# Optimization experiments

Measured on AMD Instinct MI355X. Metric: run time of the kernel, lower is better.

## Reference

```python
import jax, jax.numpy as jnp
import numpy as np

N_STREAMS = 4
HIDDEN = 1024
SINKHORN_ITERS = 20
TAU = 0.05
EPS = 1e-6
RMS_EPS = 1e-8


def rms_norm(x, weight):
    # x: [T, d] fp32
    rms = jnp.mean(x * x, axis=-1, keepdims=True)
    return x * jax.lax.rsqrt(rms + RMS_EPS) * weight


def sinkhorn_log(logits, n_iters=SINKHORN_ITERS, tau=TAU):
    # logits: [T, n, n] -> doubly-stochastic [T, n, n]
    Z = logits / tau
    u0 = jnp.zeros(Z.shape[:-1], Z.dtype)  # [T, n]
    v0 = jnp.zeros_like(u0)

    def body(i, uv):
        u, v = uv
        u = -jax.nn.logsumexp(Z + v[..., None, :], axis=-1)
        v = -jax.nn.logsumexp(Z + u[..., :, None], axis=-2)
        return (u, v)

    u, v = jax.lax.fori_loop(0, n_iters, body, (u0, v0))
    return jnp.exp(Z + u[..., :, None] + v[..., None, :])


def setup_inputs() -> dict:
    key = jax.random.key(0)
    ks = jax.random.split(key, 6)
    d = N_STREAMS * HIDDEN
    x_streams = jax.random.normal(ks[0], (4, 2048, N_STREAMS, HIDDEN), dtype=jnp.float32)
    scale = 1.0 / np.sqrt(d)
    return {
        "x_streams": x_streams,
        "rms_weight": jnp.ones((d,), jnp.float32),
        "W_pre": jax.random.normal(ks[1], (N_STREAMS, d), jnp.float32) * scale,
        "W_post": jax.random.normal(ks[2], (N_STREAMS, d), jnp.float32) * scale,
        "W_res": jax.random.normal(ks[3], (N_STREAMS * N_STREAMS, d), jnp.float32) * scale,
        "bias_pre": jnp.zeros((N_STREAMS,), jnp.float32),
        "bias_post": jnp.zeros((N_STREAMS,), jnp.float32),
        "bias_res": jnp.zeros((N_STREAMS * N_STREAMS,), jnp.float32),
        "alpha_pre": jnp.full((1,), 0.01, jnp.float32),
        "alpha_post": jnp.full((1,), 0.01, jnp.float32),
        "alpha_res": jnp.full((1,), 0.01, jnp.float32),
        "W_sub": jax.random.normal(ks[4], (HIDDEN, HIDDEN), jnp.float32) * (1.0 / np.sqrt(HIDDEN)),
    }


def reference(x_streams, rms_weight, W_pre, W_post, W_res, bias_pre, bias_post,
              bias_res, alpha_pre, alpha_post, alpha_res, W_sub):
    B, S, n, C = x_streams.shape
    d = n * C
    x_flat = x_streams.reshape(B * S, d).astype(jnp.float32)
    x_norm = rms_norm(x_flat, rms_weight)

    H_pre = jax.nn.sigmoid(alpha_pre * (x_norm @ W_pre.T) + bias_pre)        # [T, n]
    H_post = 2.0 * jax.nn.sigmoid(alpha_post * (x_norm @ W_post.T) + bias_post)
    H_res = sinkhorn_log((alpha_res * (x_norm @ W_res.T) + bias_res).reshape(B * S, n, n))

    H_pre = H_pre.reshape(B, S, n)
    H_post = H_post.reshape(B, S, n)
    H_res = H_res.reshape(B, S, n, n)

    H_pre_w = H_pre / (jnp.sum(H_pre, axis=-1, keepdims=True) + EPS)
    H_post_w = H_post / (jnp.sum(H_post, axis=-1, keepdims=True) + EPS)

    # pre-aggregate streams -> single stream
    x_layer = jnp.einsum('bsnc,bsn->bsc', x_streams, H_pre_w)
    # sublayer: bias-free linear
    y = x_layer @ W_sub.T                                                    # [B, S, C]
    # broadcast sublayer output back to streams
    y_expanded = H_post_w[..., None] * y[:, :, None, :]                      # [B, S, n, C]
    # doubly-stochastic residual stream mixing
    x_mixed = jnp.einsum('bsic,bsoi->bsoc', x_streams, H_res)
    return x_mixed + y_expanded
```

## Files before the change

kernel.cpp:

```cpp
#include <hip/hip_runtime.h>

#define NTOK 8192
#define D 4096
#define CH 1024

typedef __attribute__((ext_vector_type(8))) short short8v;
typedef __attribute__((ext_vector_type(4))) float float4v;
typedef __attribute__((ext_vector_type(4))) unsigned short ushort4v;

static __device__ __forceinline__ unsigned short f2bf(float f) {
  unsigned int u = __float_as_uint(f);
  u += 0x7fff + ((u >> 16) & 1);
  return (unsigned short)(u >> 16);
}

static __device__ __forceinline__ void async_cp16(const void* g, void* l) {
  __builtin_amdgcn_global_load_lds((__attribute__((address_space(1))) void*)g,
                                   (__attribute__((address_space(3))) void*)l,
                                   16, 0, 0);
}

__global__ __launch_bounds__(512, 4) void gates_kernel(
    const float* __restrict__ x, const float* __restrict__ rms_w,
    const float* __restrict__ Wpre, const float* __restrict__ Wpost,
    const float* __restrict__ Wres, const float* __restrict__ bpre,
    const float* __restrict__ bpost, const float* __restrict__ bres,
    const float* __restrict__ apre, const float* __restrict__ apost,
    const float* __restrict__ ares, const float* __restrict__ Wsub,
    unsigned short* __restrict__ Wb, float* __restrict__ gates_out,
    unsigned short* __restrict__ xlayer) {
  __shared__ float xbuf[4][4096];
  __shared__ float logits_lds[4][24];
  __shared__ float sq_lds[4];
  __shared__ float s_lds[4];
  __shared__ float hpre_lds[4][4];

  const int tid = threadIdx.x;
  const int lane = tid & 63;
  const int w = tid >> 6;
  const int tok0 = blockIdx.x * 4;

  {
    const int t = w >> 1;
    const int c0 = (w & 1) * 2048;
    const float* src = x + (size_t)(tok0 + t) * D + c0 + lane * 4;
#pragma unroll
    for (int j = 0; j < 8; ++j)
      async_cp16(src + j * 256, (void*)&xbuf[t][c0 + j * 256]);
  }

  if (blockIdx.x < 1024) {
    int i = blockIdx.x * 1024 + tid * 2;
    float2 v = *(const float2*)(Wsub + i);
    unsigned int packed = (unsigned int)f2bf(v.x) | ((unsigned int)f2bf(v.y) << 16);
    *(unsigned int*)(Wb + i) = packed;
  }

  const float* Wp[3];
#pragma unroll
  for (int g = 0; g < 3; ++g) {
    int gg = w * 3 + g;
    Wp[g] = (gg < 4) ? (Wpre + gg * D)
          : (gg < 8) ? (Wpost + (gg - 4) * D)
                     : (Wres + (gg - 8) * D);
  }

  float acc[3][4];
#pragma unroll
  for (int g = 0; g < 3; ++g)
#pragma unroll
    for (int t = 0; t < 4; ++t) acc[g][t] = 0.f;
  float sq = 0.f;

  __syncthreads();

#pragma unroll 4
  for (int chk = 0; chk < 16; ++chk) {
    const int cb = chk * 256 + lane * 4;
    float4 w4[3];
#pragma unroll
    for (int g = 0; g < 3; ++g) w4[g] = *(const float4*)(Wp[g] + cb);
    float4 r4 = *(const float4*)(rms_w + cb);
#pragma unroll
    for (int t = 0; t < 4; ++t) {
      float4 xv = *(const float4*)(&xbuf[t][cb]);
      if (w == (t << 1))
        sq += xv.x * xv.x + xv.y * xv.y + xv.z * xv.z + xv.w * xv.w;
      float4 xr;
      xr.x = xv.x * r4.x; xr.y = xv.y * r4.y; xr.z = xv.z * r4.z; xr.w = xv.w * r4.w;
#pragma unroll
      for (int g = 0; g < 3; ++g)
        acc[g][t] += xr.x * w4[g].x + xr.y * w4[g].y + xr.z * w4[g].z + xr.w * w4[g].w;
    }
  }

#pragma unroll
  for (int g = 0; g < 3; ++g)
#pragma unroll
    for (int t = 0; t < 4; ++t) {
      float v = acc[g][t];
      for (int off = 32; off > 0; off >>= 1) v += __shfl_xor(v, off, 64);
      if (lane == 0) logits_lds[t][w * 3 + g] = v;
    }
  if ((w & 1) == 0) {
    float v = sq;
    for (int off = 32; off > 0; off >>= 1) v += __shfl_xor(v, off, 64);
    if (lane == 0) sq_lds[w >> 1] = v;
  }
  __syncthreads();

  if (tid < 4) {
    const int t = tid;
    float s = rsqrtf(sq_lds[t] * (1.0f / 4096.0f) + 1e-8f);
    s_lds[t] = s;
    float a_pre = apre[0], a_post = apost[0];

    float hp[4];
    float sum_p = 1e-6f;
#pragma unroll
    for (int i = 0; i < 4; ++i) {
      float z = a_pre * (s * logits_lds[t][i]) + bpre[i];
      hp[i] = 1.0f / (1.0f + __expf(-z));
      sum_p += hp[i];
    }
    float inv_p = 1.0f / sum_p;
#pragma unroll
    for (int i = 0; i < 4; ++i) hpre_lds[t][i] = hp[i] * inv_p;

    float* go = gates_out + (size_t)(tok0 + t) * 20;
    float hq[4];
    float sum_q = 1e-6f;
#pragma unroll
    for (int i = 0; i < 4; ++i) {
      float z = a_post * (s * logits_lds[t][4 + i]) + bpost[i];
      hq[i] = 2.0f / (1.0f + __expf(-z));
      sum_q += hq[i];
    }
    float inv_q = 1.0f / sum_q;
#pragma unroll
    for (int i = 0; i < 4; ++i) go[i] = hq[i] * inv_q;
  }
  __syncthreads();

  auto phB = [&](int s) {
    const int t = s >> 8;
    const int c4 = (s & 255) * 4;
    const float h0 = hpre_lds[t][0], h1 = hpre_lds[t][1];
    const float h2 = hpre_lds[t][2], h3 = hpre_lds[t][3];
    const float4 x0 = *(const float4*)&xbuf[t][c4];
    const float4 x1 = *(const float4*)&xbuf[t][1024 + c4];
    const float4 x2 = *(const float4*)&xbuf[t][2048 + c4];
    const float4 x3 = *(const float4*)&xbuf[t][3072 + c4];
    ushort4v o;
    o.x = f2bf(h0 * x0.x + h1 * x1.x + h2 * x2.x + h3 * x3.x);
    o.y = f2bf(h0 * x0.y + h1 * x1.y + h2 * x2.y + h3 * x3.y);
    o.z = f2bf(h0 * x0.z + h1 * x1.z + h2 * x2.z + h3 * x3.z);
    o.w = f2bf(h0 * x0.w + h1 * x1.w + h2 * x2.w + h3 * x3.w);
    *(ushort4v*)(xlayer + (size_t)(tok0 + t) * CH + c4) = o;
  };

  if (w == 0) {
    if (lane < 16) {
      const int t = lane >> 2;
      const int r = lane & 3;
      const float s = s_lds[t];
      const float a_res = ares[0];
      float Zrow[4], Zcol[4];
#pragma unroll
      for (int j = 0; j < 4; ++j) {
        Zrow[j] = (a_res * (s * logits_lds[t][8 + r * 4 + j]) + bres[r * 4 + j]) * 20.0f;
        Zcol[j] = (a_res * (s * logits_lds[t][8 + j * 4 + r]) + bres[j * 4 + r]) * 20.0f;
      }
      float u = 0.f, v = 0.f;
      const int base = t << 2;
      for (int it = 0; it < 20; ++it) {
        float v0 = __shfl(v, base + 0, 64), v1 = __shfl(v, base + 1, 64);
        float v2 = __shfl(v, base + 2, 64), v3 = __shfl(v, base + 3, 64);
        float a0 = Zrow[0] + v0, a1 = Zrow[1] + v1, a2 = Zrow[2] + v2, a3 = Zrow[3] + v3;
        float m = fmaxf(fmaxf(a0, a1), fmaxf(a2, a3));
        float sm = __expf(a0 - m) + __expf(a1 - m) + __expf(a2 - m) + __expf(a3 - m);
        u = -(m + __logf(sm));
        float u0 = __shfl(u, base + 0, 64), u1 = __shfl(u, base + 1, 64);
        float u2 = __shfl(u, base + 2, 64), u3 = __shfl(u, base + 3, 64);
        float b0 = Zcol[0] + u0, b1 = Zcol[1] + u1, b2 = Zcol[2] + u2, b3 = Zcol[3] + u3;
        float m2 = fmaxf(fmaxf(b0, b1), fmaxf(b2, b3));
        float sm2 = __expf(b0 - m2) + __expf(b1 - m2) + __expf(b2 - m2) + __expf(b3 - m2);
        v = -(m2 + __logf(sm2));
      }
      float v0 = __shfl(v, base + 0, 64), v1 = __shfl(v, base + 1, 64);
      float v2 = __shfl(v, base + 2, 64), v3 = __shfl(v, base + 3, 64);
      float* go = gates_out + (size_t)(tok0 + t) * 20;
      go[4 + r * 4 + 0] = __expf(Zrow[0] + u + v0);
      go[4 + r * 4 + 1] = __expf(Zrow[1] + u + v1);
      go[4 + r * 4 + 2] = __expf(Zrow[2] + u + v2);
      go[4 + r * 4 + 3] = __expf(Zrow[3] + u + v3);
    }
    phB(896 + lane);
    phB(960 + lane);
  } else {
    phB(tid - 64);
    phB(tid + 384);
  }
}

__global__ __launch_bounds__(256, 2) void gemm_epi(
    const unsigned short* __restrict__ A,
    const unsigned short* __restrict__ B,
    const float* __restrict__ x,
    const float* __restrict__ gates,
    float* __restrict__ out) {
  __shared__ __align__(16) unsigned short stg[32768];
  __shared__ float hpost_sm[128][4];
  __shared__ float hres_sm[128][16];

  const int tid = threadIdx.x;
  const int lane = tid & 63;
  const int w = tid >> 6;
  const int n0 = blockIdx.x * 128;
  const int m0 = blockIdx.y * 128;

  {
    const int r = tid >> 1, half = tid & 1;
    const float* gp = gates + (size_t)(m0 + r) * 20 + half * 10;
#pragma unroll
    for (int j = 0; j < 10; ++j) {
      int jj = half * 10 + j;
      float v = gp[j];
      if (jj < 4) hpost_sm[r][jj] = v;
      else        hres_sm[r][jj - 4] = v;
    }
  }

  float4v accf[4][4];
#pragma unroll
  for (int mi = 0; mi < 4; ++mi)
#pragma unroll
    for (int ni = 0; ni < 4; ++ni) {
      accf[mi][ni].x = 0.f; accf[mi][ni].y = 0.f;
      accf[mi][ni].z = 0.f; accf[mi][ni].w = 0.f;
    }

  const int wm = (w >> 1) * 64;
  const int wn = (w & 1) * 64;
  const int srow = lane >> 3;
  const int sslot = lane & 7;

#define STAGE(KT, BUF)                                                        \
  {                                                                           \
    const int k0s = (KT) * 64;                                                \
    unsigned short* As = stg + (BUF) * 8192;                                  \
    unsigned short* Bs = stg + 16384 + (BUF) * 8192;                          \
    _Pragma("unroll")                                                         \
    for (int i = 0; i < 4; ++i) {                                             \
      int chunk = w * 4 + i;                                                  \
      int row = chunk * 8 + srow;                                             \
      int qg = sslot ^ (row & 7);                                             \
      async_cp16(A + (size_t)(m0 + row) * 1024 + k0s + qg * 8,                \
                 (void*)(As + chunk * 512));                                  \
      async_cp16(B + (size_t)(n0 + row) * 1024 + k0s + qg * 8,                \
                 (void*)(Bs + chunk * 512));                                  \
    }                                                                         \
  }

  STAGE(0, 0);
  __syncthreads();

  for (int kt = 0; kt < 16; ++kt) {
    const int cur = kt & 1;
    if (kt < 15) STAGE(kt + 1, cur ^ 1);
    const unsigned short* As = stg + cur * 8192;
    const unsigned short* Bs = stg + 16384 + cur * 8192;
#pragma unroll
    for (int kk = 0; kk < 2; ++kk) {
      short8v a[4], b[4];
#pragma unroll
      for (int mi = 0; mi < 4; ++mi) {
        int row = wm + mi * 16 + (lane & 15);
        int q = (kk * 4 + (lane >> 4)) ^ (row & 7);
        a[mi] = *(const short8v*)(As + row * 64 + q * 8);
      }
#pragma unroll
      for (int ni = 0; ni < 4; ++ni) {
        int row = wn + ni * 16 + (lane & 15);
        int q = (kk * 4 + (lane >> 4)) ^ (row & 7);
        b[ni] = *(const short8v*)(Bs + row * 64 + q * 8);
      }
#pragma unroll
      for (int mi = 0; mi < 4; ++mi)
#pragma unroll
        for (int ni = 0; ni < 4; ++ni)
          accf[mi][ni] = __builtin_amdgcn_mfma_f32_16x16x32_bf16(
              a[mi], b[ni], accf[mi][ni], 0, 0, 0);
    }
    __syncthreads();
  }

  const int rg = (lane >> 4) * 4;
  const int cl = lane & 15;
#pragma unroll
  for (int mi = 0; mi < 4; ++mi) {
#pragma unroll
    for (int r = 0; r < 4; ++r) {
      const int row = wm + mi * 16 + rg + r;
      const size_t t = (size_t)(m0 + row);
      const float4 hq = *(const float4*)(&hpost_sm[row][0]);
      const float4 h0 = *(const float4*)(&hres_sm[row][0]);
      const float4 h1 = *(const float4*)(&hres_sm[row][4]);
      const float4 h2 = *(const float4*)(&hres_sm[row][8]);
      const float4 h3 = *(const float4*)(&hres_sm[row][12]);
      const float* xp = x + t * 4096 + n0 + wn + cl;
      float* op = out + t * 4096 + n0 + wn + cl;
#pragma unroll
      for (int ni = 0; ni < 4; ++ni) {
        const int c = ni * 16;
        float x0 = xp[c], x1 = xp[c + 1024], x2 = xp[c + 2048], x3 = xp[c + 3072];
        float y = accf[mi][ni][r];
        op[c]        = x0 * h0.x + x1 * h0.y + x2 * h0.z + x3 * h0.w + hq.x * y;
        op[c + 1024] = x0 * h1.x + x1 * h1.y + x2 * h1.z + x3 * h1.w + hq.y * y;
        op[c + 2048] = x0 * h2.x + x1 * h2.y + x2 * h2.z + x3 * h2.w + hq.z * y;
        op[c + 3072] = x0 * h3.x + x1 * h3.y + x2 * h3.z + x3 * h3.w + hq.w * y;
      }
    }
  }
}

extern "C" void kernel_launch(void* const* d_in, const int* in_sizes, int n_in,
                              void* d_out, int out_size, void* d_ws, size_t ws_size,
                              hipStream_t stream) {
  const float* x     = (const float*)d_in[0];
  const float* rms_w = (const float*)d_in[1];
  const float* Wpre  = (const float*)d_in[2];
  const float* Wpost = (const float*)d_in[3];
  const float* Wres  = (const float*)d_in[4];
  const float* bpre  = (const float*)d_in[5];
  const float* bpost = (const float*)d_in[6];
  const float* bres  = (const float*)d_in[7];
  const float* apre  = (const float*)d_in[8];
  const float* apost = (const float*)d_in[9];
  const float* ares  = (const float*)d_in[10];
  const float* Wsub  = (const float*)d_in[11];
  float* out = (float*)d_out;

  char* ws = (char*)d_ws;
  float* gates           = (float*)ws;
  unsigned short* Wb     = (unsigned short*)(ws + (1 << 20));
  unsigned short* xlayer = (unsigned short*)(ws + (4 << 20));

  gates_kernel<<<2048, 512, 0, stream>>>(x, rms_w, Wpre, Wpost, Wres, bpre,
                                         bpost, bres, apre, apost, ares,
                                         Wsub, Wb, gates, xlayer);
  gemm_epi<<<dim3(8, 64), 256, 0, stream>>>(xlayer, Wb, x, gates, out);
}
```

Measured before the change: 375.9 us.

## Process eight tokens per gates block with bf16 LDS staging of x

The gates kernel now handles 8 tokens per block instead of 4, halving the grid. Each row of x is loaded synchronously, converted to bf16 into LDS, and its sum of squares is computed at load time. The RMS weight is folded into the gate weights once per chunk, so each weight load is reused across twice as many tokens. This cuts redundant weight-matrix traffic and LDS footprint but drops the async copy, gives fewer blocks for latency hiding, and makes the gate logits and x_layer less precise because x is rounded to bf16 before the dot products.

```diff
diff --git a/kernel.cpp b/kernel.cpp
--- a/kernel.cpp
+++ b/kernel.cpp
@@ -12,6 +12,10 @@
   unsigned int u = __float_as_uint(f);
   u += 0x7fff + ((u >> 16) & 1);
   return (unsigned short)(u >> 16);
+}
+
+static __device__ __forceinline__ float bf2f(unsigned short u) {
+  return __uint_as_float(((unsigned int)u) << 16);
 }
 
 static __device__ __forceinline__ void async_cp16(const void* g, void* l) {
@@ -29,31 +33,38 @@
     const float* __restrict__ ares, const float* __restrict__ Wsub,
     unsigned short* __restrict__ Wb, float* __restrict__ gates_out,
     unsigned short* __restrict__ xlayer) {
-  __shared__ float xbuf[4][4096];
-  __shared__ float logits_lds[4][24];
-  __shared__ float sq_lds[4];
-  __shared__ float s_lds[4];
-  __shared__ float hpre_lds[4][4];
+  __shared__ unsigned short xb[8][4096];
+  __shared__ float logits_lds[8][24];
+  __shared__ float sq_lds[8];
+  __shared__ float s_lds[8];
+  __shared__ float hpre_lds[8][4];
 
   const int tid = threadIdx.x;
   const int lane = tid & 63;
   const int w = tid >> 6;
-  const int tok0 = blockIdx.x * 4;
+  const int tok0 = blockIdx.x * 8;
 
   {
-    const int t = w >> 1;
-    const int c0 = (w & 1) * 2048;
-    const float* src = x + (size_t)(tok0 + t) * D + c0 + lane * 4;
-#pragma unroll
-    for (int j = 0; j < 8; ++j)
-      async_cp16(src + j * 256, (void*)&xbuf[t][c0 + j * 256]);
-  }
-
-  if (blockIdx.x < 1024) {
     int i = blockIdx.x * 1024 + tid * 2;
     float2 v = *(const float2*)(Wsub + i);
     unsigned int packed = (unsigned int)f2bf(v.x) | ((unsigned int)f2bf(v.y) << 16);
     *(unsigned int*)(Wb + i) = packed;
+  }
+
+  {
+    const float* src = x + (size_t)(tok0 + w) * D + lane * 4;
+    float sq = 0.f;
+#pragma unroll
+    for (int j = 0; j < 16; ++j) {
+      float4 v = *(const float4*)(src + j * 256);
+      sq += v.x * v.x + v.y * v.y + v.z * v.z + v.w * v.w;
+      uint2 p;
+      p.x = (unsigned int)f2bf(v.x) | ((unsigned int)f2bf(v.y) << 16);
+      p.y = (unsigned int)f2bf(v.z) | ((unsigned int)f2bf(v.w) << 16);
+      *(uint2*)(&xb[w][j * 256 + lane * 4]) = p;
+    }
+    for (int off = 32; off > 0; off >>= 1) sq += __shfl_xor(sq, off, 64);
+    if (lane == 0) sq_lds[w] = sq;
   }
 
   const float* Wp[3];
@@ -65,51 +76,46 @@
                      : (Wres + (gg - 8) * D);
   }
 
-  float acc[3][4];
+  float acc[3][8];
 #pragma unroll
   for (int g = 0; g < 3; ++g)
 #pragma unroll
-    for (int t = 0; t < 4; ++t) acc[g][t] = 0.f;
-  float sq = 0.f;
+    for (int t = 0; t < 8; ++t) acc[g][t] = 0.f;
 
   __syncthreads();
 
 #pragma unroll 4
   for (int chk = 0; chk < 16; ++chk) {
     const int cb = chk * 256 + lane * 4;
-    float4 w4[3];
-#pragma unroll
-    for (int g = 0; g < 3; ++g) w4[g] = *(const float4*)(Wp[g] + cb);
     float4 r4 = *(const float4*)(rms_w + cb);
-#pragma unroll
-    for (int t = 0; t < 4; ++t) {
-      float4 xv = *(const float4*)(&xbuf[t][cb]);
-      if (w == (t << 1))
-        sq += xv.x * xv.x + xv.y * xv.y + xv.z * xv.z + xv.w * xv.w;
-      float4 xr;
-      xr.x = xv.x * r4.x; xr.y = xv.y * r4.y; xr.z = xv.z * r4.z; xr.w = xv.w * r4.w;
+    float4 wr[3];
+#pragma unroll
+    for (int g = 0; g < 3; ++g) {
+      float4 w4 = *(const float4*)(Wp[g] + cb);
+      wr[g].x = w4.x * r4.x; wr[g].y = w4.y * r4.y;
+      wr[g].z = w4.z * r4.z; wr[g].w = w4.w * r4.w;
+    }
+#pragma unroll
+    for (int t = 0; t < 8; ++t) {
+      ushort4v xv = *(const ushort4v*)(&xb[t][cb]);
+      float x0 = bf2f(xv.x), x1 = bf2f(xv.y), x2 = bf2f(xv.z), x3 = bf2f(xv.w);
 #pragma unroll
       for (int g = 0; g < 3; ++g)
-        acc[g][t] += xr.x * w4[g].x + xr.y * w4[g].y + xr.z * w4[g].z + xr.w * w4[g].w;
+        acc[g][t] += x0 * wr[g].x + x1 * wr[g].y + x2 * wr[g].z + x3 * wr[g].w;
     }
   }
 
 #pragma unroll
   for (int g = 0; g < 3; ++g)
 #pragma unroll
-    for (int t = 0; t < 4; ++t) {
+    for (int t = 0; t < 8; ++t) {
       float v = acc[g][t];
       for (int off = 32; off > 0; off >>= 1) v += __shfl_xor(v, off, 64);
       if (lane == 0) logits_lds[t][w * 3 + g] = v;
     }
-  if ((w & 1) == 0) {
-    float v = sq;
-    for (int off = 32; off > 0; off >>= 1) v += __shfl_xor(v, off, 64);
-    if (lane == 0) sq_lds[w >> 1] = v;
-  }
   __syncthreads();
 
-  if (tid < 4) {
+  if (tid < 8) {
     const int t = tid;
     float s = rsqrtf(sq_lds[t] * (1.0f / 4096.0f) + 1e-8f);
     s_lds[t] = s;
@@ -142,25 +148,25 @@
   }
   __syncthreads();
 
-  auto phB = [&](int s) {
-    const int t = s >> 8;
-    const int c4 = (s & 255) * 4;
+  auto phB = [&](int sI) {
+    const int t = sI >> 8;
+    const int c4 = (sI & 255) * 4;
     const float h0 = hpre_lds[t][0], h1 = hpre_lds[t][1];
     const float h2 = hpre_lds[t][2], h3 = hpre_lds[t][3];
-    const float4 x0 = *(const float4*)&xbuf[t][c4];
-    const float4 x1 = *(const float4*)&xbuf[t][1024 + c4];
-    const float4 x2 = *(const float4*)&xbuf[t][2048 + c4];
-    const float4 x3 = *(const float4*)&xbuf[t][3072 + c4];
+    ushort4v v0 = *(const ushort4v*)&xb[t][c4];
+    ushort4v v1 = *(const ushort4v*)&xb[t][1024 + c4];
+    ushort4v v2 = *(const ushort4v*)&xb[t][2048 + c4];
+    ushort4v v3 = *(const ushort4v*)&xb[t][3072 + c4];
     ushort4v o;
-    o.x = f2bf(h0 * x0.x + h1 * x1.x + h2 * x2.x + h3 * x3.x);
-    o.y = f2bf(h0 * x0.y + h1 * x1.y + h2 * x2.y + h3 * x3.y);
-    o.z = f2bf(h0 * x0.z + h1 * x1.z + h2 * x2.z + h3 * x3.z);
-    o.w = f2bf(h0 * x0.w + h1 * x1.w + h2 * x2.w + h3 * x3.w);
+    o.x = f2bf(h0 * bf2f(v0.x) + h1 * bf2f(v1.x) + h2 * bf2f(v2.x) + h3 * bf2f(v3.x));
+    o.y = f2bf(h0 * bf2f(v0.y) + h1 * bf2f(v1.y) + h2 * bf2f(v2.y) + h3 * bf2f(v3.y));
+    o.z = f2bf(h0 * bf2f(v0.z) + h1 * bf2f(v1.z) + h2 * bf2f(v2.z) + h3 * bf2f(v3.z));
+    o.w = f2bf(h0 * bf2f(v0.w) + h1 * bf2f(v1.w) + h2 * bf2f(v2.w) + h3 * bf2f(v3.w));
     *(ushort4v*)(xlayer + (size_t)(tok0 + t) * CH + c4) = o;
   };
 
   if (w == 0) {
-    if (lane < 16) {
+    if (lane < 32) {
       const int t = lane >> 2;
       const int r = lane & 3;
       const float s = s_lds[t];
@@ -195,11 +201,12 @@
       go[4 + r * 4 + 2] = __expf(Zrow[2] + u + v2);
       go[4 + r * 4 + 3] = __expf(Zrow[3] + u + v3);
     }
-    phB(896 + lane);
-    phB(960 + lane);
+#pragma unroll
+    for (int i = 0; i < 4; ++i) phB(1792 + i * 64 + lane);
   } else {
-    phB(tid - 64);
-    phB(tid + 384);
+    const int b = tid - 64;
+#pragma unroll
+    for (int i = 0; i < 4; ++i) phB(b + i * 448);
   }
 }
 
@@ -346,7 +353,7 @@
   unsigned short* Wb     = (unsigned short*)(ws + (1 << 20));
   unsigned short* xlayer = (unsigned short*)(ws + (4 << 20));
 
-  gates_kernel<<<2048, 512, 0, stream>>>(x, rms_w, Wpre, Wpost, Wres, bpre,
+  gates_kernel<<<1024, 512, 0, stream>>>(x, rms_w, Wpre, Wpost, Wres, bpre,
                                          bpost, bres, apre, apost, ares,
                                          Wsub, Wb, gates, xlayer);
   gemm_epi<<<dim3(8, 64), 256, 0, stream>>>(xlayer, Wb, x, gates, out);
```

Result: faster. 362.8 us (-3.5%).
